# Kernel optimization log

Measured on AMD Instinct MI355X. Metric: run time of the kernel, lower is better.

## Reference

```python
import jax, jax.numpy as jnp
import numpy as np

B, S, DIN, DOUT = 4, 512, 4096, 10240


def setup_inputs() -> dict:
    key = jax.random.key(0)
    k1, k2, k3, k4 = jax.random.split(key, 4)
    # Activation in fp16, as the module casts input to self.dtype (fp16)
    input_tensor = jax.random.normal(k1, (B, S, DIN), dtype=jnp.float32).astype(jnp.float16)
    # weight emulates fp8 e4m3 storage; values here stand in for the dequant source
    weight = jax.random.normal(k2, (DOUT, DIN), dtype=jnp.float32) * 0.02
    # per-output-channel scale, stored fp32
    weight_scale = jax.random.uniform(k3, (DOUT, 1), dtype=jnp.float32, minval=0.5, maxval=1.5)
    bias = (jax.random.normal(k4, (DOUT,), dtype=jnp.float32) * 0.02).astype(jnp.float16)
    return {"input_tensor": input_tensor, "weight": weight, "weight_scale": weight_scale, "bias": bias}


def reference(input_tensor, weight, weight_scale, bias):
    # Dequantize: fp8 weight -> fp16, multiply by per-row scale (cast to fp16)
    w16 = weight.astype(jnp.float16) * weight_scale.astype(jnp.float16)  # [DOUT, DIN]
    # F.linear: x @ W^T + b, all in fp16
    out = jnp.einsum('bsi,oi->bso', input_tensor, w16) + bias  # [B, S, DOUT]
    return out
```

## Files before the change

### kernel.cpp

```cpp
#include <hip/hip_runtime.h>
#include <hip/hip_fp16.h>

typedef _Float16 half8 __attribute__((ext_vector_type(8)));
typedef float f32x4 __attribute__((ext_vector_type(4)));

constexpr int M = 2048;
constexpr int N = 10240;
constexpr int K = 4096;

constexpr long A_VEC = (long)M * K / 8;
constexpr long W_VEC = (long)N * K / 8;

__global__ __launch_bounds__(256)
void prep_kernel(const float* __restrict__ A, const float* __restrict__ W,
                 const float* __restrict__ Wsc,
                 _Float16* __restrict__ Ah, _Float16* __restrict__ Wh) {
    const long total = A_VEC + W_VEC;
    for (long i = (long)blockIdx.x * blockDim.x + threadIdx.x; i < total;
         i += (long)gridDim.x * blockDim.x) {
        if (i < A_VEC) {
            const long base = i * 8;
            const float4 a0 = ((const float4*)(A + base))[0];
            const float4 a1 = ((const float4*)(A + base))[1];
            half8 h;
            h[0] = (_Float16)a0.x; h[1] = (_Float16)a0.y;
            h[2] = (_Float16)a0.z; h[3] = (_Float16)a0.w;
            h[4] = (_Float16)a1.x; h[5] = (_Float16)a1.y;
            h[6] = (_Float16)a1.z; h[7] = (_Float16)a1.w;
            *(half8*)(Ah + base) = h;
        } else {
            const long base = (i - A_VEC) * 8;
            const int row = (int)(base >> 12);
            const _Float16 s = (_Float16)Wsc[row];
            const float4 w0 = ((const float4*)(W + base))[0];
            const float4 w1 = ((const float4*)(W + base))[1];
            half8 h;
            h[0] = (_Float16)w0.x * s; h[1] = (_Float16)w0.y * s;
            h[2] = (_Float16)w0.z * s; h[3] = (_Float16)w0.w * s;
            h[4] = (_Float16)w1.x * s; h[5] = (_Float16)w1.y * s;
            h[6] = (_Float16)w1.z * s; h[7] = (_Float16)w1.w * s;
            *(half8*)(Wh + base) = h;
        }
    }
}

constexpr int BM = 256, BN = 320, BK = 64;
constexpr int AELE = BM * BK;
constexpr int BELE = BN * BK;
constexpr int NT = K / BK;

#define BAR()   asm volatile("s_barrier" ::: "memory")
#define LGKM0() asm volatile("s_waitcnt lgkmcnt(0)" ::: "memory")

__device__ __forceinline__ half8 lds_rd(const _Float16* base, int row, int eo) {
    const int ps = (eo >> 3) ^ (row & 7);
    return *(const half8*)(base + row * BK + ps * 8);
}

__global__ __launch_bounds__(512, 2)
void qgemm256x320v4_kernel(const _Float16* __restrict__ Ag,
                           const _Float16* __restrict__ Wg,
                           const float*    __restrict__ bias,
                           float*          __restrict__ C)
{
    __shared__ _Float16 AsF[2 * AELE];
    __shared__ _Float16 BsF[2 * BELE];

    const int orig = blockIdx.x;
    const int wgid = (orig & 7) * 32 + (orig >> 3);
    const int m0 = (wgid & 7) * BM;
    const int n0 = (wgid >> 3) * BN;

    const int tid  = threadIdx.x;
    const int lane = tid & 63;
    const int w    = tid >> 6;
    const int wm   = w >> 2;
    const int wn   = w & 3;
    const int fr   = lane & 15;
    const int fkE  = (lane >> 4) * 8;

    const int trow  = tid >> 3;
    const int swcol = (((tid & 7) ^ (trow & 7))) * 8;

    auto stage_a = [&](int b, int u, int kcol) {
        const _Float16* src = Ag + (size_t)(m0 + u * 64 + trow) * K + (kcol + swcol);
        __builtin_amdgcn_global_load_lds(
            (const __attribute__((address_space(1))) void*)src,
            (__attribute__((address_space(3))) void*)(AsF + b * AELE + u * 4096 + tid * 8),
            16, 0, 0);
    };
    auto stage_b = [&](int b, int u, int kcol) {
        const _Float16* src = Wg + (size_t)(n0 + u * 64 + trow) * K + (kcol + swcol);
        __builtin_amdgcn_global_load_lds(
            (const __attribute__((address_space(1))) void*)src,
            (__attribute__((address_space(3))) void*)(BsF + b * BELE + u * 4096 + tid * 8),
            16, 0, 0);
    };

    f32x4 acc[8][5];
#pragma unroll
    for (int i = 0; i < 8; ++i)
#pragma unroll
        for (int j = 0; j < 5; ++j)
            acc[i][j] = (f32x4){0.f, 0.f, 0.f, 0.f};

#pragma unroll
    for (int u = 0; u < 4; ++u) stage_a(0, u, 0);
#pragma unroll
    for (int u = 0; u < 5; ++u) stage_b(0, u, 0);
#pragma unroll
    for (int u = 0; u < 4; ++u) stage_a(1, u, BK);
#pragma unroll
    for (int u = 0; u < 5; ++u) stage_b(1, u, BK);
    asm volatile("s_waitcnt vmcnt(9)" ::: "memory");
    BAR();

    const int rowA = wm * 128 + fr;
    const int rowB = wn * 80 + fr;

#pragma unroll 1
    for (int t = 0; t < NT; ++t) {
        const int cur = t & 1;
        const _Float16* Ab = AsF + cur * AELE;
        const _Float16* Bb = BsF + cur * BELE;
        const bool pf2 = (t + 2 < NT);
        const int k2 = (t + 2) * BK;

        {
            half8 b0[5], a0[8];
#pragma unroll
            for (int cb = 0; cb < 5; ++cb)
                b0[cb] = lds_rd(Bb, rowB + cb * 16, fkE);
#pragma unroll
            for (int rb = 0; rb < 8; ++rb)
                a0[rb] = lds_rd(Ab, rowA + rb * 16, fkE);
            __builtin_amdgcn_s_setprio(1);
#pragma unroll
            for (int cb = 0; cb < 5; ++cb)
#pragma unroll
                for (int rb = 0; rb < 8; ++rb)
                    acc[rb][cb] = __builtin_amdgcn_mfma_f32_16x16x32_f16(
                        a0[rb], b0[cb], acc[rb][cb], 0, 0, 0);
            __builtin_amdgcn_s_setprio(0);
        }

        half8 b1[5], a1[8];
#pragma unroll
        for (int cb = 0; cb < 5; ++cb)
            b1[cb] = lds_rd(Bb, rowB + cb * 16, 32 + fkE);
#pragma unroll
        for (int rb = 0; rb < 8; ++rb)
            a1[rb] = lds_rd(Ab, rowA + rb * 16, 32 + fkE);
        __builtin_amdgcn_s_setprio(1);
#pragma unroll
        for (int cb = 0; cb < 5; ++cb)
#pragma unroll
            for (int rb = 0; rb < 4; ++rb)
                acc[rb][cb] = __builtin_amdgcn_mfma_f32_16x16x32_f16(
                    a1[rb], b1[cb], acc[rb][cb], 0, 0, 0);
        __builtin_amdgcn_s_setprio(0);
        LGKM0();
        BAR();

        if (pf2) {
#pragma unroll
            for (int u = 0; u < 4; ++u) stage_a(cur, u, k2);
#pragma unroll
            for (int u = 0; u < 5; ++u) stage_b(cur, u, k2);
        }
        __builtin_amdgcn_s_setprio(1);
#pragma unroll
        for (int cb = 0; cb < 5; ++cb)
#pragma unroll
            for (int rb = 4; rb < 8; ++rb)
                acc[rb][cb] = __builtin_amdgcn_mfma_f32_16x16x32_f16(
                    a1[rb], b1[cb], acc[rb][cb], 0, 0, 0);
        __builtin_amdgcn_s_setprio(0);
        if (pf2) asm volatile("s_waitcnt vmcnt(9)" ::: "memory");
        else     asm volatile("s_waitcnt vmcnt(0)" ::: "memory");
        BAR();
    }

    float bb[5];
#pragma unroll
    for (int j = 0; j < 5; ++j)
        bb[j] = bias[n0 + wn * 80 + j * 16 + fr];
#pragma unroll
    for (int i = 0; i < 8; ++i) {
        const int row = m0 + wm * 128 + i * 16 + (lane >> 4) * 4;
#pragma unroll
        for (int j = 0; j < 5; ++j) {
            const int col = n0 + wn * 80 + j * 16 + fr;
#pragma unroll
            for (int r = 0; r < 4; ++r)
                C[(size_t)(row + r) * N + col] =
                    (float)(_Float16)(acc[i][j][r] + bb[j]);
        }
    }
}

__global__ __launch_bounds__(256, 2)
void qlinear_fused_kernel(const float* __restrict__ A, const float* __restrict__ W,
                          const float* __restrict__ Wsc, const float* __restrict__ bias,
                          float* __restrict__ C)
{
    __shared__ _Float16 As[128][64];
    __shared__ _Float16 Bs[128][64];

    const int nwg  = (M / 128) * (N / 128);
    const int orig = blockIdx.x;
    const int wgid = (orig & 7) * (nwg >> 3) + (orig >> 3);
    const int brow = wgid & (M / 128 - 1);
    const int bcol = wgid / (M / 128);
    const int m0 = brow * 128;
    const int n0 = bcol * 128;

    const int t    = threadIdx.x;
    const int lane = t & 63;
    const int wave = t >> 6;
    const int wr = (wave >> 1) * 64;
    const int wc = (wave & 1) * 64;
    const int fr = lane & 15;
    const int fk = (lane >> 4) * 8;
    const int srow = t >> 3;
    const int scol = (t & 7) * 8;

    _Float16 hs[4];
#pragma unroll
    for (int p = 0; p < 4; ++p)
        hs[p] = (_Float16)Wsc[n0 + srow + p * 32];

    f32x4 acc[4][4];
#pragma unroll
    for (int i = 0; i < 4; ++i)
#pragma unroll
        for (int j = 0; j < 4; ++j)
            acc[i][j] = (f32x4){0.f, 0.f, 0.f, 0.f};

    for (int k0 = 0; k0 < K; k0 += 64) {
        __syncthreads();
#pragma unroll
        for (int c = 0; c < 4; ++c) {
            const int rl = c * 32 + srow;
            const float* asrc = A + (size_t)(m0 + rl) * K + (k0 + scol);
            const float4 a0 = ((const float4*)asrc)[0];
            const float4 a1 = ((const float4*)asrc)[1];
            half8 av;
            av[0] = (_Float16)a0.x; av[1] = (_Float16)a0.y;
            av[2] = (_Float16)a0.z; av[3] = (_Float16)a0.w;
            av[4] = (_Float16)a1.x; av[5] = (_Float16)a1.y;
            av[6] = (_Float16)a1.z; av[7] = (_Float16)a1.w;
            *(half8*)&As[rl][scol] = av;
        }
#pragma unroll
        for (int p = 0; p < 4; ++p) {
            const int nl = srow + p * 32;
            const float* wsrc = W + (size_t)(n0 + nl) * K + (k0 + scol);
            const float4 w0 = ((const float4*)wsrc)[0];
            const float4 w1 = ((const float4*)wsrc)[1];
            half8 hv;
            hv[0] = (_Float16)w0.x * hs[p]; hv[1] = (_Float16)w0.y * hs[p];
            hv[2] = (_Float16)w0.z * hs[p]; hv[3] = (_Float16)w0.w * hs[p];
            hv[4] = (_Float16)w1.x * hs[p]; hv[5] = (_Float16)w1.y * hs[p];
            hv[6] = (_Float16)w1.z * hs[p]; hv[7] = (_Float16)w1.w * hs[p];
            *(half8*)&Bs[nl][scol] = hv;
        }
        __syncthreads();
#pragma unroll
        for (int kk = 0; kk < 64; kk += 32) {
            half8 av[4], bv[4];
#pragma unroll
            for (int i = 0; i < 4; ++i)
                av[i] = *(const half8*)&As[wr + i * 16 + fr][kk + fk];
#pragma unroll
            for (int j = 0; j < 4; ++j)
                bv[j] = *(const half8*)&Bs[wc + j * 16 + fr][kk + fk];
#pragma unroll
            for (int i = 0; i < 4; ++i)
#pragma unroll
                for (int j = 0; j < 4; ++j)
                    acc[i][j] = __builtin_amdgcn_mfma_f32_16x16x32_f16(
                        av[i], bv[j], acc[i][j], 0, 0, 0);
        }
    }
#pragma unroll
    for (int i = 0; i < 4; ++i) {
        const int row = m0 + wr + i * 16 + (lane >> 4) * 4;
#pragma unroll
        for (int j = 0; j < 4; ++j) {
            const int col = n0 + wc + j * 16 + fr;
            const float bbf = bias[col];
#pragma unroll
            for (int r = 0; r < 4; ++r)
                C[(size_t)(row + r) * N + col] =
                    (float)(_Float16)(acc[i][j][r] + bbf);
        }
    }
}

extern "C" void kernel_launch(void* const* d_in, const int* in_sizes, int n_in,
                              void* d_out, int out_size, void* d_ws, size_t ws_size,
                              hipStream_t stream) {
    const float* A    = (const float*)d_in[0];
    const float* W    = (const float*)d_in[1];
    const float* Wsc  = (const float*)d_in[2];
    const float* bias = (const float*)d_in[3];
    float* C = (float*)d_out;

    const size_t a_bytes = (size_t)M * K * sizeof(_Float16);
    const size_t w_bytes = (size_t)N * K * sizeof(_Float16);

    if (ws_size >= a_bytes + w_bytes) {
        _Float16* Ah = (_Float16*)d_ws;
        _Float16* Wh = (_Float16*)((char*)d_ws + a_bytes);
        prep_kernel<<<dim3(2048), dim3(256), 0, stream>>>(A, W, Wsc, Ah, Wh);
        const int nwg = (M / BM) * (N / BN);
        qgemm256x320v4_kernel<<<dim3(nwg), dim3(512), 0, stream>>>(Ah, Wh, bias, C);
    } else {
        const int nwg = (M / 128) * (N / 128);
        qlinear_fused_kernel<<<dim3(nwg), dim3(256), 0, stream>>>(A, W, Wsc, bias, C);
    }
}
```

Baseline: 201.4 us.

## Switch GEMM inner loop to 32x32x16 MFMA with 4x2 wave layout

Replaces the 16x16x32 f16 MFMA tiles with 32x32x16 MFMA instructions and regroups the eight waves as 4x2 (64x160 per wave) instead of 2x4 (128x80). Each wave now issues fewer, larger MFMAs and fewer LDS fragment reads per K-step, which lowers instruction count and LDS traffic per flop. The epilogue is rewritten for the 32x32 accumulator lane-to-row mapping. The larger MFMA has different latency and scheduling behaviour, and the uneven split of the second half-step around the barrier may change how well MFMAs overlap the prefetch.

```diff
diff --git a/kernel.cpp b/kernel.cpp
--- a/kernel.cpp
+++ b/kernel.cpp
@@ -2,7 +2,7 @@
 #include <hip/hip_fp16.h>
 
 typedef _Float16 half8 __attribute__((ext_vector_type(8)));
-typedef float f32x4 __attribute__((ext_vector_type(4)));
+typedef float f32x16 __attribute__((ext_vector_type(16)));
 
 constexpr int M = 2048;
 constexpr int N = 10240;
@@ -58,10 +58,10 @@
 }
 
 __global__ __launch_bounds__(512, 2)
-void qgemm256x320v4_kernel(const _Float16* __restrict__ Ag,
-                           const _Float16* __restrict__ Wg,
-                           const float*    __restrict__ bias,
-                           float*          __restrict__ C)
+void qgemm32x32_kernel(const _Float16* __restrict__ Ag,
+                       const _Float16* __restrict__ Wg,
+                       const float*    __restrict__ bias,
+                       float*          __restrict__ C)
 {
     __shared__ _Float16 AsF[2 * AELE];
     __shared__ _Float16 BsF[2 * BELE];
@@ -74,10 +74,10 @@
     const int tid  = threadIdx.x;
     const int lane = tid & 63;
     const int w    = tid >> 6;
-    const int wm   = w >> 2;
-    const int wn   = w & 3;
-    const int fr   = lane & 15;
-    const int fkE  = (lane >> 4) * 8;
+    const int wm   = w >> 1;
+    const int wn   = w & 1;
+    const int l31  = lane & 31;
+    const int kq   = (lane >> 5) * 8;
 
     const int trow  = tid >> 3;
     const int swcol = (((tid & 7) ^ (trow & 7))) * 8;
@@ -97,12 +97,14 @@
             16, 0, 0);
     };
 
-    f32x4 acc[8][5];
-#pragma unroll
-    for (int i = 0; i < 8; ++i)
+    f32x16 acc[2][5];
+#pragma unroll
+    for (int i = 0; i < 2; ++i)
 #pragma unroll
         for (int j = 0; j < 5; ++j)
-            acc[i][j] = (f32x4){0.f, 0.f, 0.f, 0.f};
+#pragma unroll
+            for (int r = 0; r < 16; ++r)
+                acc[i][j][r] = 0.f;
 
 #pragma unroll
     for (int u = 0; u < 4; ++u) stage_a(0, u, 0);
@@ -115,8 +117,8 @@
     asm volatile("s_waitcnt vmcnt(9)" ::: "memory");
     BAR();
 
-    const int rowA = wm * 128 + fr;
-    const int rowB = wn * 80 + fr;
+    const int rowA = wm * 64 + l31;
+    const int rowB = wn * 160 + l31;
 
 #pragma unroll 1
     for (int t = 0; t < NT; ++t) {
@@ -127,37 +129,47 @@
         const int k2 = (t + 2) * BK;
 
         {
-            half8 b0[5], a0[8];
+            half8 b0[5][2], a0[2][2];
 #pragma unroll
             for (int cb = 0; cb < 5; ++cb)
-                b0[cb] = lds_rd(Bb, rowB + cb * 16, fkE);
-#pragma unroll
-            for (int rb = 0; rb < 8; ++rb)
-                a0[rb] = lds_rd(Ab, rowA + rb * 16, fkE);
+#pragma unroll
+                for (int ks = 0; ks < 2; ++ks)
+                    b0[cb][ks] = lds_rd(Bb, rowB + cb * 32, ks * 16 + kq);
+#pragma unroll
+            for (int rb = 0; rb < 2; ++rb)
+#pragma unroll
+                for (int ks = 0; ks < 2; ++ks)
+                    a0[rb][ks] = lds_rd(Ab, rowA + rb * 32, ks * 16 + kq);
             __builtin_amdgcn_s_setprio(1);
 #pragma unroll
             for (int cb = 0; cb < 5; ++cb)
 #pragma unroll
-                for (int rb = 0; rb < 8; ++rb)
-                    acc[rb][cb] = __builtin_amdgcn_mfma_f32_16x16x32_f16(
-                        a0[rb], b0[cb], acc[rb][cb], 0, 0, 0);
+                for (int rb = 0; rb < 2; ++rb)
+#pragma unroll
+                    for (int ks = 0; ks < 2; ++ks)
+                        acc[rb][cb] = __builtin_amdgcn_mfma_f32_32x32x16_f16(
+                            a0[rb][ks], b0[cb][ks], acc[rb][cb], 0, 0, 0);
             __builtin_amdgcn_s_setprio(0);
         }
 
-        half8 b1[5], a1[8];
+        half8 b1[5][2], a1[2][2];
 #pragma unroll
         for (int cb = 0; cb < 5; ++cb)
-            b1[cb] = lds_rd(Bb, rowB + cb * 16, 32 + fkE);
-#pragma unroll
-        for (int rb = 0; rb < 8; ++rb)
-            a1[rb] = lds_rd(Ab, rowA + rb * 16, 32 + fkE);
+#pragma unroll
+            for (int ks = 0; ks < 2; ++ks)
+                b1[cb][ks] = lds_rd(Bb, rowB + cb * 32, 32 + ks * 16 + kq);
+#pragma unroll
+        for (int rb = 0; rb < 2; ++rb)
+#pragma unroll
+            for (int ks = 0; ks < 2; ++ks)
+                a1[rb][ks] = lds_rd(Ab, rowA + rb * 32, 32 + ks * 16 + kq);
         __builtin_amdgcn_s_setprio(1);
 #pragma unroll
         for (int cb = 0; cb < 5; ++cb)
 #pragma unroll
-            for (int rb = 0; rb < 4; ++rb)
-                acc[rb][cb] = __builtin_amdgcn_mfma_f32_16x16x32_f16(
-                    a1[rb], b1[cb], acc[rb][cb], 0, 0, 0);
+            for (int ks = 0; ks < 2; ++ks)
+                acc[0][cb] = __builtin_amdgcn_mfma_f32_32x32x16_f16(
+                    a1[0][ks], b1[cb][ks], acc[0][cb], 0, 0, 0);
         __builtin_amdgcn_s_setprio(0);
         LGKM0();
         BAR();
@@ -172,9 +184,9 @@
 #pragma unroll
         for (int cb = 0; cb < 5; ++cb)
 #pragma unroll
-            for (int rb = 4; rb < 8; ++rb)
-                acc[rb][cb] = __builtin_amdgcn_mfma_f32_16x16x32_f16(
-                    a1[rb], b1[cb], acc[rb][cb], 0, 0, 0);
+            for (int ks = 0; ks < 2; ++ks)
+                acc[1][cb] = __builtin_amdgcn_mfma_f32_32x32x16_f16(
+                    a1[1][ks], b1[cb][ks], acc[1][cb], 0, 0, 0);
         __builtin_amdgcn_s_setprio(0);
         if (pf2) asm volatile("s_waitcnt vmcnt(9)" ::: "memory");
         else     asm volatile("s_waitcnt vmcnt(0)" ::: "memory");
@@ -184,17 +196,19 @@
     float bb[5];
 #pragma unroll
     for (int j = 0; j < 5; ++j)
-        bb[j] = bias[n0 + wn * 80 + j * 16 + fr];
-#pragma unroll
-    for (int i = 0; i < 8; ++i) {
-        const int row = m0 + wm * 128 + i * 16 + (lane >> 4) * 4;
+        bb[j] = bias[n0 + wn * 160 + j * 32 + l31];
+    const int rbase = m0 + wm * 64 + 4 * (lane >> 5);
+#pragma unroll
+    for (int i = 0; i < 2; ++i) {
 #pragma unroll
         for (int j = 0; j < 5; ++j) {
-            const int col = n0 + wn * 80 + j * 16 + fr;
-#pragma unroll
-            for (int r = 0; r < 4; ++r)
-                C[(size_t)(row + r) * N + col] =
+            const int col = n0 + wn * 160 + j * 32 + l31;
+#pragma unroll
+            for (int r = 0; r < 16; ++r) {
+                const int row = rbase + i * 32 + (r & 3) + 8 * (r >> 2);
+                C[(size_t)row * N + col] =
                     (float)(_Float16)(acc[i][j][r] + bb[j]);
+            }
         }
     }
 }
@@ -204,6 +218,7 @@
                           const float* __restrict__ Wsc, const float* __restrict__ bias,
                           float* __restrict__ C)
 {
+    typedef float f32x4 __attribute__((ext_vector_type(4)));
     __shared__ _Float16 As[128][64];
     __shared__ _Float16 Bs[128][64];
 
@@ -315,7 +330,7 @@
         _Float16* Wh = (_Float16*)((char*)d_ws + a_bytes);
         prep_kernel<<<dim3(2048), dim3(256), 0, stream>>>(A, W, Wsc, Ah, Wh);
         const int nwg = (M / BM) * (N / BN);
-        qgemm256x320v4_kernel<<<dim3(nwg), dim3(512), 0, stream>>>(Ah, Wh, bias, C);
+        qgemm32x32_kernel<<<dim3(nwg), dim3(512), 0, stream>>>(Ah, Wh, bias, C);
     } else {
         const int nwg = (M / 128) * (N / 128);
         qlinear_fused_kernel<<<dim3(nwg), dim3(256), 0, stream>>>(A, W, Wsc, bias, C);
```

Result: slower. 253.5 us (+25.9%).
